# Kernel tuning notes

Measured on AMD Instinct MI355X. Metric: run time of the kernel, lower is better.

The kernel has to match this reference:

```python
import jax, jax.numpy as jnp
import numpy as np
from jax import lax

# sign binarization to {-1,+1} with straight-through estimator (standard BNN binarizePM1)
@jax.custom_vjp
def binarize(x):
    return jnp.where(x >= 0, 1.0, -1.0).astype(x.dtype)

def _bin_fwd(x):
    return binarize(x), None

def _bin_bwd(_, g):
    return (g,)  # straight-through

binarize.defvjp(_bin_fwd, _bin_bwd)

def conv2d(x, w, b):
    # NCHW, OIHW, 3x3, stride 1, pad 1
    y = lax.conv_general_dilated(x, w, window_strides=(1, 1), padding=((1, 1), (1, 1)),
                                 dimension_numbers=('NCHW', 'OIHW', 'NCHW'))
    return y + b[None, :, None, None]

def maxpool2(x):
    return lax.reduce_window(x, -jnp.inf, lax.max, (1, 1, 2, 2), (1, 1, 2, 2), 'VALID')

def bn(x, gamma, beta, mean, var, eps=1e-5):
    # inference-mode batchnorm; broadcasts over channel axis 1 (4D) or feature axis 1 (2D)
    if x.ndim == 4:
        shp = (1, -1, 1, 1)
    else:
        shp = (1, -1)
    inv = gamma * lax.rsqrt(var + eps)
    return x * inv.reshape(shp) + (beta - mean * inv).reshape(shp)

def setup_inputs() -> dict:
    key = jax.random.key(0)
    ks = jax.random.split(key, 16)
    B = 4096
    d = {}
    d['x'] = jax.random.normal(ks[0], (B, 1, 28, 28), jnp.float32)
    d['conv1_w'] = jax.random.normal(ks[1], (64, 1, 3, 3), jnp.float32) * 0.1
    d['conv1_b'] = jax.random.normal(ks[2], (64,), jnp.float32) * 0.01
    d['conv2_w'] = jax.random.normal(ks[3], (64, 64, 3, 3), jnp.float32) * 0.05
    d['conv2_b'] = jax.random.normal(ks[4], (64,), jnp.float32) * 0.01
    d['fc1_w'] = jax.random.normal(ks[5], (2048, 7 * 7 * 64), jnp.float32) * 0.02
    d['fc1_b'] = jax.random.normal(ks[6], (2048,), jnp.float32) * 0.01
    d['fc2_w'] = jax.random.normal(ks[7], (10, 2048), jnp.float32) * 0.02
    d['fc2_b'] = jax.random.normal(ks[8], (10,), jnp.float32) * 0.01
    for i, (name, c) in enumerate([('bn1', 64), ('bn2', 64), ('bn3', 2048)]):
        d[name + '_gamma'] = jnp.ones((c,), jnp.float32)
        d[name + '_beta'] = jnp.zeros((c,), jnp.float32)
        d[name + '_mean'] = jax.random.normal(ks[9 + i], (c,), jnp.float32) * 0.1
        d[name + '_var'] = jax.random.uniform(ks[12 + i], (c,), jnp.float32, 0.5, 1.5)
    d['scale'] = jnp.array([1e-5], jnp.float32)
    return d

def reference(x, conv1_w, conv1_b, conv2_w, conv2_b, fc1_w, fc1_b, fc2_w, fc2_b,
              bn1_gamma, bn1_beta, bn1_mean, bn1_var,
              bn2_gamma, bn2_beta, bn2_mean, bn2_var,
              bn3_gamma, bn3_beta, bn3_mean, bn3_var, scale):
    h = conv2d(x, binarize(conv1_w), conv1_b)          # [B,64,28,28]
    h = maxpool2(h)                                    # [B,64,14,14]
    h = bn(h, bn1_gamma, bn1_beta, bn1_mean, bn1_var)
    h = jnp.clip(h, -1.0, 1.0)                         # hardtanh
    h = binarize(h)                                    # qact1
    h = conv2d(h, binarize(conv2_w), conv2_b)          # [B,64,14,14]
    h = maxpool2(h)                                    # [B,64,7,7]
    h = bn(h, bn2_gamma, bn2_beta, bn2_mean, bn2_var)
    h = jnp.clip(h, -1.0, 1.0)
    h = binarize(h)
    h = h.reshape(h.shape[0], -1)                      # [B,3136]
    h = h @ binarize(fc1_w).T + fc1_b                  # [B,2048]
    h = bn(h, bn3_gamma, bn3_beta, bn3_mean, bn3_var)
    h = jnp.clip(h, -1.0, 1.0)
    h = binarize(h)
    h = h @ binarize(fc2_w).T + fc2_b                  # [B,10]
    return h * scale
```

## Files before the change

kernel.cpp:

```cpp
#include <hip/hip_runtime.h>
#include <stdint.h>

typedef unsigned long long ULL;


__global__ void prep_sgn1(const float* __restrict__ w1, float* __restrict__ sgn1) {
    int t = blockIdx.x * 256 + threadIdx.x;
    if (t < 576) sgn1[t] = (w1[t] >= 0.f) ? 1.f : -1.f;
}

__global__ void prep_pack_small(const float* __restrict__ w2, const float* __restrict__ fc2w,
                                ULL* __restrict__ wb2, ULL* __restrict__ wbf2) {
    int wave = threadIdx.x >> 6, lane = threadIdx.x & 63;
    int W = blockIdx.x * 4 + wave;
    if (W < 576) {
        int co = W / 9, tap = W - co * 9;
        ULL wd = __ballot(w2[(co * 64 + lane) * 9 + tap] >= 0.f);
        if (lane == 0) wb2[W] = wd;
    } else if (W < 576 + 320) {
        int idx = W - 576;
        int n = idx >> 5, k = idx & 31;
        ULL wd = __ballot(fc2w[n * 2048 + k * 64 + lane] >= 0.f);
        if (lane == 0) wbf2[idx] = wd;
    }
}

__global__ __launch_bounds__(256) void prep_pack_fc1(const float* __restrict__ fc1w,
                                                     ULL* __restrict__ wbT) {
    __shared__ float rows[4 * 3136];
    int t = threadIdx.x;
    const float* src = fc1w + (size_t)blockIdx.x * 4 * 3136;
    for (int i = t; i < 4 * 3136; i += 256) rows[i] = src[i];
    __syncthreads();
    int wave = t >> 6, lane = t & 63;
    int n = blockIdx.x * 4 + wave;
    const float* r = rows + wave * 3136 + lane * 49;
    for (int p = 0; p < 49; ++p) {
        ULL wd = __ballot(r[p] >= 0.f);
        if (lane == 0) wbT[p * 2048 + n] = wd;
    }
}

__global__ __launch_bounds__(256) void k1_conv1(const float* __restrict__ x,
        const float* __restrict__ sgn1, const float* __restrict__ b1,
        const float* __restrict__ g, const float* __restrict__ be,
        const float* __restrict__ mu, const float* __restrict__ va,
        ULL* __restrict__ qact1) {
    __shared__ double invd[64], cd[64], bd[64];
    int b = blockIdx.x, t = threadIdx.x;
    if (t < 64) {
        double iv = (double)g[t] / sqrt((double)va[t] + 1e-5);
        invd[t] = iv;
        cd[t]  = (double)be[t] - (double)mu[t] * iv;
        bd[t]  = (double)b1[t];
    }
    __syncthreads();
    if (t < 196) {
        int py = t / 14, px = t - py * 14;
        int y0 = 2 * py - 1, x0 = 2 * px - 1;
        float patch[4][4];
        const float* xb = x + (size_t)b * 784;
        #pragma unroll
        for (int r = 0; r < 4; ++r) {
            int y = y0 + r;
            #pragma unroll
            for (int c = 0; c < 4; ++c) {
                int xx = x0 + c;
                patch[r][c] = (y >= 0 && y < 28 && xx >= 0 && xx < 28) ? xb[y * 28 + xx] : 0.f;
            }
        }
        ULL mask = 0;
        for (int co = 0; co < 64; ++co) {
            const float* s = sgn1 + co * 9;
            float a00 = 0.f, a01 = 0.f, a10 = 0.f, a11 = 0.f;
            #pragma unroll
            for (int ky = 0; ky < 3; ++ky) {
                #pragma unroll
                for (int kx = 0; kx < 3; ++kx) {
                    float sv = s[ky * 3 + kx];
                    a00 = fmaf(patch[ky][kx],         sv, a00);
                    a01 = fmaf(patch[ky][kx + 1],     sv, a01);
                    a10 = fmaf(patch[ky + 1][kx],     sv, a10);
                    a11 = fmaf(patch[ky + 1][kx + 1], sv, a11);
                }
            }
            float m = fmaxf(fmaxf(a00, a01), fmaxf(a10, a11));
            double v  = (double)m + bd[co];
            double tt = v * invd[co] + cd[co];
            mask |= (ULL)(tt >= 0.0) << co;
        }
        qact1[(size_t)b * 196 + t] = mask;
    }
}

__global__ __launch_bounds__(448) void k2_conv2(const ULL* __restrict__ qact1,
        const ULL* __restrict__ wb2, const float* __restrict__ b2,
        const float* __restrict__ g, const float* __restrict__ be,
        const float* __restrict__ mu, const float* __restrict__ va,
        ULL* __restrict__ qact2) {
    __shared__ ULL ap[16][16];
    int b = blockIdx.x, t = threadIdx.x;
    int pr = t >> 6, lane = t & 63;
    if (t < 256) ap[t >> 4][t & 15] = 0ULL;
    __syncthreads();
    if (t < 196) ap[1 + t / 14][1 + t % 14] = qact1[(size_t)b * 196 + t];

    ULL wk[9];
    #pragma unroll
    for (int k = 0; k < 9; ++k) wk[k] = wb2[lane * 9 + k];
    int pw[9];
    #pragma unroll
    for (int k = 0; k < 9; ++k) pw[k] = 64 - 2 * (int)__popcll(wk[k]);
    double iv   = (double)g[lane] / sqrt((double)va[lane] + 1e-5);
    double cc   = (double)be[lane] - (double)mu[lane] * iv;
    double bias = (double)b2[lane];

    int corr[2][3];
    #pragma unroll
    for (int j = 0; j < 2; ++j) {
        bool tpad = (pr == 0 && j == 0);
        bool bpad = (pr == 6 && j == 1);
        #pragma unroll
        for (int cls = 0; cls < 3; ++cls) {
            int cacc = 0;
            #pragma unroll
            for (int r = 0; r < 3; ++r) {
                #pragma unroll
                for (int k = 0; k < 3; ++k) {
                    bool pad = (r == 0 && tpad) || (r == 2 && bpad) ||
                               (k == 0 && cls == 0) || (k == 2 && cls == 2);
                    if (pad) cacc += pw[r * 3 + k];
                }
            }
            corr[j][cls] = cacc;
        }
    }
    __syncthreads();

    ULL win[4][4];
    #pragma unroll
    for (int r = 0; r < 4; ++r) {
        win[r][0] = ap[2 * pr + r][0];
        win[r][1] = ap[2 * pr + r][1];
    }
    for (int px = 0; px < 7; ++px) {
        #pragma unroll
        for (int r = 0; r < 4; ++r) {
            win[r][2] = ap[2 * pr + r][2 * px + 2];
            win[r][3] = ap[2 * pr + r][2 * px + 3];
        }
        int s00 = 0, s01 = 0, s10 = 0, s11 = 0;
        #pragma unroll
        for (int r = 0; r < 3; ++r) {
            #pragma unroll
            for (int k = 0; k < 3; ++k) {
                ULL w = wk[r * 3 + k];
                s00 += (int)__popcll(win[r][k]         ^ w);
                s01 += (int)__popcll(win[r][k + 1]     ^ w);
                s10 += (int)__popcll(win[r + 1][k]     ^ w);
                s11 += (int)__popcll(win[r + 1][k + 1] ^ w);
            }
        }
        int clsL = (px == 0) ? 0 : 1, clsR = (px == 6) ? 2 : 1;
        int d00 = 576 - 2 * s00 - corr[0][clsL];
        int d01 = 576 - 2 * s01 - corr[0][clsR];
        int d10 = 576 - 2 * s10 - corr[1][clsL];
        int d11 = 576 - 2 * s11 - corr[1][clsR];
        int m = max(max(d00, d01), max(d10, d11));
        double tt = ((double)m + bias) * iv + cc;
        ULL word = __ballot(tt >= 0.0);
        if (lane == 0) qact2[(size_t)b * 49 + pr * 7 + px] = word;
        #pragma unroll
        for (int r = 0; r < 4; ++r) {
            win[r][0] = win[r][2];
            win[r][1] = win[r][3];
        }
    }
}

__global__ __launch_bounds__(256) void k3_fc1(const ULL* __restrict__ qact2,
        const ULL* __restrict__ wbT, const float* __restrict__ fb,
        const float* __restrict__ g, const float* __restrict__ be,
        const float* __restrict__ mu, const float* __restrict__ va,
        ULL* __restrict__ hbits) {
    __shared__ ULL xs[784];
    int t = threadIdx.x, wave = t >> 6, lane = t & 63;
    int b0 = blockIdx.x * 16;
    int gidx = blockIdx.y * 4 + wave;
    int n = gidx * 64 + lane;
    for (int i = t; i < 784; i += 256) xs[i] = qact2[(size_t)b0 * 49 + i];
    double iv   = (double)g[n] / sqrt((double)va[n] + 1e-5);
    double cc   = (double)be[n] - (double)mu[n] * iv;
    double bias = (double)fb[n];
    __syncthreads();
    int acc[16];
    #pragma unroll
    for (int i = 0; i < 16; ++i) acc[i] = 0;
    for (int p = 0; p < 49; ++p) {
        ULL w = wbT[p * 2048 + n];
        #pragma unroll
        for (int i = 0; i < 16; ++i)
            acc[i] += (int)__popcll(xs[i * 49 + p] ^ w);
    }
    #pragma unroll
    for (int i = 0; i < 16; ++i) {
        int dot = 3136 - 2 * acc[i];
        double tt = ((double)dot + bias) * iv + cc;
        ULL word = __ballot(tt >= 0.0);
        if (lane == 0) hbits[(size_t)(b0 + i) * 32 + gidx] = word;
    }
}

__global__ __launch_bounds__(256) void k4_fc2(const ULL* __restrict__ hbits,
        const ULL* __restrict__ wbf2, const float* __restrict__ b2,
        const float* __restrict__ scale, float* __restrict__ out, int total) {
    int gid = blockIdx.x * 256 + threadIdx.x;
    if (gid >= total) return;
    int b = gid / 10, n = gid - b * 10;
    const ULL* h = hbits + (size_t)b * 32;
    const ULL* w = wbf2 + n * 32;
    int acc = 0;
    #pragma unroll
    for (int k = 0; k < 32; ++k) acc += (int)__popcll(h[k] ^ w[k]);
    int dot = 2048 - 2 * acc;
    double v = ((double)dot + (double)b2[n]) * (double)scale[0];
    out[gid] = (float)v;
}

extern "C" void kernel_launch(void* const* d_in, const int* in_sizes, int n_in,
                              void* d_out, int out_size, void* d_ws, size_t ws_size,
                              hipStream_t stream) {
    const float* x      = (const float*)d_in[0];
    const float* w1     = (const float*)d_in[1];
    const float* b1     = (const float*)d_in[2];
    const float* w2     = (const float*)d_in[3];
    const float* b2     = (const float*)d_in[4];
    const float* fc1w   = (const float*)d_in[5];
    const float* fc1b   = (const float*)d_in[6];
    const float* fc2w   = (const float*)d_in[7];
    const float* fc2b   = (const float*)d_in[8];
    const float* g1 = (const float*)d_in[9],  *be1 = (const float*)d_in[10],
               *mu1 = (const float*)d_in[11], *va1 = (const float*)d_in[12];
    const float* g2 = (const float*)d_in[13], *be2 = (const float*)d_in[14],
               *mu2 = (const float*)d_in[15], *va2 = (const float*)d_in[16];
    const float* g3 = (const float*)d_in[17], *be3 = (const float*)d_in[18],
               *mu3 = (const float*)d_in[19], *va3 = (const float*)d_in[20];
    const float* scale = (const float*)d_in[21];
    float* out = (float*)d_out;

    int B = in_sizes[0] / 784;

    char* ws = (char*)d_ws;
    ULL* qact1 = (ULL*)(ws);
    ULL* qact2 = (ULL*)(ws + (size_t)B * 196 * 8);
    ULL* hbits = (ULL*)(ws + (size_t)B * 245 * 8);
    char* wsw  = ws + (size_t)B * 277 * 8;
    ULL* wb2   = (ULL*)(wsw);
    ULL* wbT   = (ULL*)(wsw + 576 * 8);
    ULL* wbf2  = (ULL*)(wsw + 576 * 8 + 49 * 2048 * 8);
    float* sgn1 = (float*)(wsw + 576 * 8 + 49 * 2048 * 8 + 320 * 8);

    prep_sgn1<<<3, 256, 0, stream>>>(w1, sgn1);
    prep_pack_small<<<224, 256, 0, stream>>>(w2, fc2w, wb2, wbf2);
    prep_pack_fc1<<<512, 256, 0, stream>>>(fc1w, wbT);

    k1_conv1<<<B, 256, 0, stream>>>(x, sgn1, b1, g1, be1, mu1, va1, qact1);
    k2_conv2<<<B, 448, 0, stream>>>(qact1, wb2, b2, g2, be2, mu2, va2, qact2);
    k3_fc1<<<dim3(B / 16, 8), 256, 0, stream>>>(qact2, wbT, fc1b, g3, be3, mu3, va3, hbits);
    int total = B * 10;
    k4_fc2<<<(total + 255) / 256, 256, 0, stream>>>(hbits, wbf2, fc2b, scale, out, total);
}
```

Baseline: 339.1 us.

## Remap conv1 so lanes own output channels and stage image transposed in LDS

conv1 previously had each thread own one pooled pixel and loop serially over all 64 output channels, building the bit mask itself. Now each lane owns one output channel, with its weights and BN constants held in registers. Each of 7 waves sweeps two pooled rows over a sliding 4x4 window read from a zero-padded, transposed LDS copy of the image, and __ballot builds the 64-bit channel mask. This raises active threads from 196 to 448 per block and removes per-channel shared-memory and global weight loads, at the cost of serial px loops and LDS reads that every lane in a wave repeats.

After: 312.9 us. 7.7% less time.

```diff
diff --git a/kernel.cpp b/kernel.cpp
--- a/kernel.cpp
+++ b/kernel.cpp
@@ -41,55 +41,69 @@
     }
 }
 
-__global__ __launch_bounds__(256) void k1_conv1(const float* __restrict__ x,
+__global__ __launch_bounds__(448) void k1_conv1(const float* __restrict__ x,
         const float* __restrict__ sgn1, const float* __restrict__ b1,
         const float* __restrict__ g, const float* __restrict__ be,
         const float* __restrict__ mu, const float* __restrict__ va,
         ULL* __restrict__ qact1) {
-    __shared__ double invd[64], cd[64], bd[64];
+    __shared__ float limg[30 * 30];
     int b = blockIdx.x, t = threadIdx.x;
-    if (t < 64) {
-        double iv = (double)g[t] / sqrt((double)va[t] + 1e-5);
-        invd[t] = iv;
-        cd[t]  = (double)be[t] - (double)mu[t] * iv;
-        bd[t]  = (double)b1[t];
-    }
-    __syncthreads();
-    if (t < 196) {
-        int py = t / 14, px = t - py * 14;
-        int y0 = 2 * py - 1, x0 = 2 * px - 1;
-        float patch[4][4];
-        const float* xb = x + (size_t)b * 784;
-        #pragma unroll
-        for (int r = 0; r < 4; ++r) {
-            int y = y0 + r;
-            #pragma unroll
-            for (int c = 0; c < 4; ++c) {
-                int xx = x0 + c;
-                patch[r][c] = (y >= 0 && y < 28 && xx >= 0 && xx < 28) ? xb[y * 28 + xx] : 0.f;
-            }
-        }
-        ULL mask = 0;
-        for (int co = 0; co < 64; ++co) {
-            const float* s = sgn1 + co * 9;
+    int wave = t >> 6, lane = t & 63;
+    for (int i = t; i < 900; i += 448) limg[i] = 0.f;
+    __syncthreads();
+    const float* xb = x + (size_t)b * 784;
+    for (int i = t; i < 784; i += 448) {
+        int y = i / 28, xx = i - y * 28;
+        limg[(xx + 1) * 30 + (y + 1)] = xb[i];
+    }
+    float w[9];
+    #pragma unroll
+    for (int k = 0; k < 9; ++k) w[k] = sgn1[lane * 9 + k];
+    double iv = (double)g[lane] / sqrt((double)va[lane] + 1e-5);
+    double cd = (double)be[lane] - (double)mu[lane] * iv;
+    double bd = (double)b1[lane];
+    __syncthreads();
+
+    #pragma unroll
+    for (int rr = 0; rr < 2; ++rr) {
+        int py = wave + rr * 7;
+        float win[4][4];
+        #pragma unroll
+        for (int c = 0; c < 2; ++c) {
+            const float2* cp = (const float2*)&limg[c * 30 + 2 * py];
+            float2 lo = cp[0], hi = cp[1];
+            win[0][c] = lo.x; win[1][c] = lo.y; win[2][c] = hi.x; win[3][c] = hi.y;
+        }
+        for (int px = 0; px < 14; ++px) {
+            #pragma unroll
+            for (int c = 0; c < 2; ++c) {
+                const float2* cp = (const float2*)&limg[(2 * px + 2 + c) * 30 + 2 * py];
+                float2 lo = cp[0], hi = cp[1];
+                win[0][2 + c] = lo.x; win[1][2 + c] = lo.y; win[2][2 + c] = hi.x; win[3][2 + c] = hi.y;
+            }
             float a00 = 0.f, a01 = 0.f, a10 = 0.f, a11 = 0.f;
             #pragma unroll
             for (int ky = 0; ky < 3; ++ky) {
                 #pragma unroll
                 for (int kx = 0; kx < 3; ++kx) {
-                    float sv = s[ky * 3 + kx];
-                    a00 = fmaf(patch[ky][kx],         sv, a00);
-                    a01 = fmaf(patch[ky][kx + 1],     sv, a01);
-                    a10 = fmaf(patch[ky + 1][kx],     sv, a10);
-                    a11 = fmaf(patch[ky + 1][kx + 1], sv, a11);
+                    float sv = w[ky * 3 + kx];
+                    a00 = fmaf(win[ky][kx],         sv, a00);
+                    a01 = fmaf(win[ky][kx + 1],     sv, a01);
+                    a10 = fmaf(win[ky + 1][kx],     sv, a10);
+                    a11 = fmaf(win[ky + 1][kx + 1], sv, a11);
                 }
             }
             float m = fmaxf(fmaxf(a00, a01), fmaxf(a10, a11));
-            double v  = (double)m + bd[co];
-            double tt = v * invd[co] + cd[co];
-            mask |= (ULL)(tt >= 0.0) << co;
-        }
-        qact1[(size_t)b * 196 + t] = mask;
+            double v  = (double)m + bd;
+            double tt = v * iv + cd;
+            ULL word = __ballot(tt >= 0.0);
+            if (lane == 0) qact1[(size_t)b * 196 + py * 14 + px] = word;
+            #pragma unroll
+            for (int r = 0; r < 4; ++r) {
+                win[r][0] = win[r][2];
+                win[r][1] = win[r][3];
+            }
+        }
     }
 }
 
@@ -264,7 +278,7 @@
     prep_pack_small<<<224, 256, 0, stream>>>(w2, fc2w, wb2, wbf2);
     prep_pack_fc1<<<512, 256, 0, stream>>>(fc1w, wbT);
 
-    k1_conv1<<<B, 256, 0, stream>>>(x, sgn1, b1, g1, be1, mu1, va1, qact1);
+    k1_conv1<<<B, 448, 0, stream>>>(x, sgn1, b1, g1, be1, mu1, va1, qact1);
     k2_conv2<<<B, 448, 0, stream>>>(qact1, wb2, b2, g2, be2, mu2, va2, qact2);
     k3_fc1<<<dim3(B / 16, 8), 256, 0, stream>>>(qact2, wbT, fc1b, g3, be3, mu3, va3, hbits);
     int total = B * 10;
```
